# Kernel tuning notes

Measured on AMD Instinct MI355X. Metric: run time of the kernel, lower is better.

The kernel has to match this reference:

```python
import jax, jax.numpy as jnp
import numpy as np

N_NODES = 50000
N_EDGES = 800000
F_IN, C1, C2 = 128, 100, 4
NEG_SLOPE = 0.2  # PyG GATConv default LeakyReLU slope


def setup_inputs() -> dict:
    key = jax.random.key(0)
    ks = jax.random.split(key, 10)
    def glorot(k, shape):
        fan = sum(shape)
        return jax.random.normal(k, shape, jnp.float32) * jnp.sqrt(2.0 / fan)
    return {
        "x": jax.random.normal(ks[0], (N_NODES, F_IN), jnp.float32),
        "edge_index": jax.random.randint(ks[1], (2, N_EDGES), 0, N_NODES, jnp.int64),
        "W1": glorot(ks[2], (F_IN, C1)),
        "att_src1": glorot(ks[3], (1, C1)),
        "att_dst1": glorot(ks[4], (1, C1)),
        "b1": jnp.zeros((C1,), jnp.float32),
        "W2": glorot(ks[5], (C1, C2)),
        "att_src2": glorot(ks[6], (1, C2)),
        "att_dst2": glorot(ks[7], (1, C2)),
        "b2": jnp.zeros((C2,), jnp.float32),
    }


def _gat_conv(x, edge_index, W, att_src, att_dst, bias):
    """PyG GATConv (heads=1, concat=True, add_self_loops=True), eval mode."""
    n = x.shape[0]
    # add self loops
    loop = jnp.arange(n, dtype=edge_index.dtype)
    src = jnp.concatenate([edge_index[0], loop])
    dst = jnp.concatenate([edge_index[1], loop])
    h = x @ W                                   # [N, C]
    a_src = (h * att_src[0]).sum(-1)            # [N]
    a_dst = (h * att_dst[0]).sum(-1)            # [N]
    e = jax.nn.leaky_relu(a_src[src] + a_dst[dst], NEG_SLOPE)  # [E+N]
    # segment softmax over destination neighborhoods
    m = jax.ops.segment_max(e, dst, num_segments=n)            # [N]
    w = jnp.exp(e - m[dst])
    denom = jax.ops.segment_sum(w, dst, num_segments=n)        # [N]
    alpha = w / denom[dst]                                     # [E+N]
    msg = h[src] * alpha[:, None]                              # [E+N, C]
    out = jax.ops.segment_sum(msg, dst, num_segments=n)        # [N, C]
    return out + bias


def reference(x, edge_index, W1, att_src1, att_dst1, b1, W2, att_src2, att_dst2, b2):
    h = _gat_conv(x, edge_index, W1, att_src1, att_dst1, b1)
    h = jax.nn.relu(h)  # dropout is identity in eval mode
    h = _gat_conv(h, edge_index, W2, att_src2, att_dst2, b2)
    return jax.nn.log_softmax(h, axis=1)
```

## Files before the change

### kernel.cpp

```cpp
#include <hip/hip_runtime.h>
#include <math.h>

#define N_NODES 50000
#define N_EDGES 800000
#define F_IN 128
#define C1 100
#define C1D 50
#define C2 4
#define NEG 0.2f
#define DEGCAP 64
#define NBUCK 196
#define BCAP 4608
#define BSTR 16
#define PA_NB 196
#define PA_CHUNK 1021
#define GEMM_NB 782
#define NB_PREP 56
#define AGG1_NB 2048
#define AGG1_NW (AGG1_NB * 4)

typedef __attribute__((ext_vector_type(8))) _Float16 f16x8;
typedef __attribute__((ext_vector_type(2))) _Float16 f16x2;
typedef __attribute__((ext_vector_type(4))) float f32x4;

__device__ __forceinline__ float leaky(float v) { return v > 0.f ? v : NEG * v; }

__device__ __forceinline__ unsigned pkh(float a, float b) {
    auto p = __builtin_amdgcn_cvt_pkrtz(a, b);
    return __builtin_bit_cast(unsigned, p);
}
__device__ __forceinline__ float h_lo(unsigned g) {
    f16x2 p = __builtin_bit_cast(f16x2, g);
    return (float)p[0];
}
__device__ __forceinline__ float h_hi(unsigned g) {
    f16x2 p = __builtin_bit_cast(f16x2, g);
    return (float)p[1];
}

__global__ __launch_bounds__(256) void k_prep(int* __restrict__ bcnt, const float* __restrict__ W1,
                                              unsigned short* __restrict__ W1h) {
    int i = blockIdx.x * 256 + threadIdx.x;
    if (i < NBUCK) bcnt[i * BSTR] = 0;
    if (i < 12800) {
        int k = i / 100, n = i - k * 100;
        _Float16 hv = (_Float16)W1[i];
        W1h[n * 128 + k] = __builtin_bit_cast(unsigned short, hv);
    } else if (i < 12800 + 12 * 128) {
        int e = i - 12800;
        int n = 100 + (e >> 7), k = e & 127;
        W1h[n * 128 + k] = 0;
    }
}

__global__ __launch_bounds__(256)
void k_gemm_scatter(const float* __restrict__ x, const unsigned short* __restrict__ W1h,
                    const float* __restrict__ as1, const float* __restrict__ ad1,
                    unsigned* __restrict__ h1b, float* __restrict__ a_src1,
                    float* __restrict__ a_dst1, const int* __restrict__ ei,
                    int* __restrict__ bcnt, unsigned* __restrict__ breg) {
    if (blockIdx.x < PA_NB) {
        __shared__ int lcnt[NBUCK];
        __shared__ int lbase[NBUCK];
        int tid = threadIdx.x;
        if (tid < NBUCK) lcnt[tid] = 0;
        __syncthreads();
        int g0 = blockIdx.x * PA_CHUNK;
        int4 s4[4], d4[4];
        int off[4][4];
        bool val[4];
#pragma unroll
        for (int it = 0; it < 4; ++it) {
            int local = it * 256 + tid;
            int g = g0 + local;
            val[it] = (local < PA_CHUNK) && (g < N_EDGES / 4);
            if (val[it]) {
                s4[it] = *(const int4*)(ei + (long)g * 4);
                d4[it] = *(const int4*)(ei + N_EDGES + (long)g * 4);
                off[it][0] = atomicAdd(&lcnt[d4[it].x >> 8], 1);
                off[it][1] = atomicAdd(&lcnt[d4[it].y >> 8], 1);
                off[it][2] = atomicAdd(&lcnt[d4[it].z >> 8], 1);
                off[it][3] = atomicAdd(&lcnt[d4[it].w >> 8], 1);
            }
        }
        __syncthreads();
        if (tid < NBUCK) {
            int c = lcnt[tid];
            lbase[tid] = c ? atomicAdd(&bcnt[tid * BSTR], c) : 0;
        }
        __syncthreads();
#pragma unroll
        for (int it = 0; it < 4; ++it) {
            if (!val[it]) continue;
            { int b = d4[it].x >> 8; int p = lbase[b] + off[it][0];
              if (p < BCAP) breg[b * BCAP + p] = ((unsigned)s4[it].x << 8) | ((unsigned)d4[it].x & 255u); }
            { int b = d4[it].y >> 8; int p = lbase[b] + off[it][1];
              if (p < BCAP) breg[b * BCAP + p] = ((unsigned)s4[it].y << 8) | ((unsigned)d4[it].y & 255u); }
            { int b = d4[it].z >> 8; int p = lbase[b] + off[it][2];
              if (p < BCAP) breg[b * BCAP + p] = ((unsigned)s4[it].z << 8) | ((unsigned)d4[it].z & 255u); }
            { int b = d4[it].w >> 8; int p = lbase[b] + off[it][3];
              if (p < BCAP) breg[b * BCAP + p] = ((unsigned)s4[it].w << 8) | ((unsigned)d4[it].w & 255u); }
        }
        return;
    }
    int half = blockIdx.x - PA_NB;
    int tid = threadIdx.x;
    int node0 = half * 64;
    int wave = tid >> 6, lane = tid & 63;
    int mrow = lane & 15;
    int quad = lane >> 4;
    int na = node0 + wave * 16 + mrow;
    bool vrow = na < N_NODES;
    const float* px = x + (long)na * F_IN + quad * 8;

    f16x8 afr[4];
#pragma unroll
    for (int kc = 0; kc < 4; ++kc) {
        float4 v0 = make_float4(0.f, 0.f, 0.f, 0.f), v1 = v0;
        if (vrow) {
            v0 = *(const float4*)(px + kc * 32);
            v1 = *(const float4*)(px + kc * 32 + 4);
        }
        union { unsigned u[4]; f16x8 h; } t;
        t.u[0] = pkh(v0.x, v0.y);
        t.u[1] = pkh(v0.z, v0.w);
        t.u[2] = pkh(v1.x, v1.y);
        t.u[3] = pkh(v1.z, v1.w);
        afr[kc] = t.h;
    }

    f32x4 acc[7];
#pragma unroll
    for (int nt = 0; nt < 7; ++nt) {
        const _Float16* pb = (const _Float16*)W1h + (nt * 16 + mrow) * 128 + quad * 8;
        f32x4 a = {0.f, 0.f, 0.f, 0.f};
#pragma unroll
        for (int kc = 0; kc < 4; ++kc) {
            f16x8 bfr = *(const f16x8*)(pb + kc * 32);
            a = __builtin_amdgcn_mfma_f32_16x16x32_f16(afr[kc], bfr, a, 0, 0, 0);
        }
        acc[nt] = a;
    }

    float ps[4] = {0.f, 0.f, 0.f, 0.f}, pd[4] = {0.f, 0.f, 0.f, 0.f};
#pragma unroll
    for (int nt = 0; nt < 7; ++nt) {
        int col = nt * 16 + mrow;
        float av = 0.f, dv = 0.f;
        if (col < C1) { av = as1[col]; dv = ad1[col]; }
#pragma unroll
        for (int r = 0; r < 4; ++r) {
            ps[r] += acc[nt][r] * av;
            pd[r] += acc[nt][r] * dv;
        }
    }
#pragma unroll
    for (int r = 0; r < 4; ++r) {
#pragma unroll
        for (int off = 1; off < 16; off <<= 1) {
            ps[r] += __shfl_xor(ps[r], off);
            pd[r] += __shfl_xor(pd[r], off);
        }
    }
    if (mrow == 0) {
#pragma unroll
        for (int r = 0; r < 4; ++r) {
            int n = node0 + wave * 16 + quad * 4 + r;
            if (n < N_NODES) { a_src1[n] = ps[r]; a_dst1[n] = pd[r]; }
        }
    }

#pragma unroll
    for (int nt = 0; nt < 7; ++nt) {
#pragma unroll
        for (int r = 0; r < 4; ++r) {
            float v = acc[nt][r];
            float o = __shfl_xor(v, 1);
            int col = nt * 16 + mrow;
            int n = node0 + wave * 16 + quad * 4 + r;
            if ((mrow & 1) == 0 && col < C1 && n < N_NODES) {
                h1b[(long)n * C1D + (col >> 1)] = pkh(v, o);
            }
        }
    }
}

__global__ __launch_bounds__(512) void k_bucket(const unsigned* __restrict__ breg,
                                                const int* __restrict__ bcnt,
                                                int* __restrict__ cnt,
                                                unsigned short* __restrict__ slots) {
    __shared__ int dcnt[256];
    int b = blockIdx.x, tid = threadIdx.x;
    if (tid < 256) dcnt[tid] = 0;
    __syncthreads();
    int n = min(bcnt[b * BSTR], BCAP);
    const unsigned* reg = breg + b * BCAP;
    for (int e = tid; e < n; e += 512) {
        unsigned p = reg[e];
        int d8 = p & 255;
        int slot = atomicAdd(&dcnt[d8], 1);
        if (slot < DEGCAP) slots[(((b << 8) + d8) << 6) + slot] = (unsigned short)(p >> 8);
    }
    __syncthreads();
    if (tid < 256) {
        int d = (b << 8) + tid;
        if (d < N_NODES) cnt[d] = dcnt[tid];
    }
}

__device__ __forceinline__ float rlanef(float v, int l) {
    return __int_as_float(__builtin_amdgcn_readlane(__float_as_int(v), l));
}

__global__ __launch_bounds__(256) void k_agg1(const unsigned* __restrict__ h1b, const float* __restrict__ a_src,
                                              const float* __restrict__ a_dst, const int* __restrict__ cnt,
                                              const unsigned short* __restrict__ slots, const float* __restrict__ b1,
                                              const float* __restrict__ W2, const float* __restrict__ as2,
                                              const float* __restrict__ ad2, float4* __restrict__ h2,
                                              float* __restrict__ a_src2, float* __restrict__ a_dst2) {
    int tid = threadIdx.x;
    int wave = tid >> 6, lane = tid & 63;
    int wid = blockIdx.x * 4 + wave;
    bool act = lane < C1D;
    int cc = act ? lane : 0;

    int d = wid;
    if (d >= N_NODES) return;
    int cnC = min(cnt[d], DEGCAP);
    int sregC = (int)slots[d * DEGCAP + lane];
    float adC = a_dst[d];
    float asdC = a_src[d];

    while (true) {
        int dn = d + AGG1_NW;
        int cnN = 0, sregN = 0; float adN = 0.f, asdN = 0.f;
        if (dn < N_NODES) {
            cnN = min(cnt[dn], DEGCAP);
            sregN = (int)slots[dn * DEGCAP + lane];
            adN = a_dst[dn];
            asdN = a_src[dn];
        }
        int cn = cnC; float ad = adC;
        float asg = a_src[sregC];
        unsigned gs = h1b[(long)d * C1D + cc];
        unsigned ga[8], gb[8];
#define LD(buf, e) { int sv_ = __builtin_amdgcn_readlane(sregC, (e)); \
                     buf = h1b[(long)sv_ * C1D + cc]; }
#define CONSUME(buf, e) if ((e) < cn) { float w_ = rlanef(wreg, (e)); \
                     accL = fmaf(h_lo(buf), w_, accL); accH = fmaf(h_hi(buf), w_, accH); }
#pragma unroll
        for (int i = 0; i < 8; ++i) LD(ga[i], i);
        float wself = __expf(leaky(asdC + ad));
        float wreg = __expf(leaky(asg + ad));
        float lsum = (lane == 0) ? wself : 0.f;
        if (lane < cn) lsum += wreg;
        float accL = wself * h_lo(gs), accH = wself * h_hi(gs);
#pragma unroll
        for (int bp = 0; bp < 4; ++bp) {
            const int b0 = 2 * bp, b1i = 2 * bp + 1;
            if (b0 * 8 >= cn) break;
            if (b1i * 8 < cn) {
#pragma unroll
                for (int i = 0; i < 8; ++i) LD(gb[i], b1i * 8 + i);
            }
#pragma unroll
            for (int i = 0; i < 8; ++i) CONSUME(ga[i], b0 * 8 + i);
            if (b1i * 8 >= cn) break;
            if ((b1i + 1) * 8 < cn) {
#pragma unroll
                for (int i = 0; i < 8; ++i) LD(ga[i], (b1i + 1) * 8 + i);
            }
#pragma unroll
            for (int i = 0; i < 8; ++i) CONSUME(gb[i], b1i * 8 + i);
        }
#undef LD
#undef CONSUME

        for (int off = 32; off; off >>= 1) lsum += __shfl_xor(lsum, off);
        float invl = 1.f / lsum;
        float p0 = 0.f, p1 = 0.f, p2 = 0.f, p3 = 0.f;
        if (act) {
            float v0 = fmaxf(accL * invl + b1[2 * lane], 0.f);
            float v1 = fmaxf(accH * invl + b1[2 * lane + 1], 0.f);
            const float* w0 = W2 + (2 * lane) * 4;
            p0 = v0 * w0[0] + v1 * w0[4];
            p1 = v0 * w0[1] + v1 * w0[5];
            p2 = v0 * w0[2] + v1 * w0[6];
            p3 = v0 * w0[3] + v1 * w0[7];
        }
        for (int off = 32; off; off >>= 1) {
            p0 += __shfl_xor(p0, off);
            p1 += __shfl_xor(p1, off);
            p2 += __shfl_xor(p2, off);
            p3 += __shfl_xor(p3, off);
        }
        if (lane == 0) {
            h2[d] = make_float4(p0, p1, p2, p3);
            a_src2[d] = p0 * as2[0] + p1 * as2[1] + p2 * as2[2] + p3 * as2[3];
            a_dst2[d] = p0 * ad2[0] + p1 * ad2[1] + p2 * ad2[2] + p3 * ad2[3];
        }
        if (dn >= N_NODES) break;
        d = dn; cnC = cnN; sregC = sregN; adC = adN; asdC = asdN;
    }
}

__global__ __launch_bounds__(256) void k_agg2(const float4* __restrict__ h2, const float* __restrict__ a_src,
                                              const float* __restrict__ a_dst, const int* __restrict__ cnt,
                                              const unsigned short* __restrict__ slots, const float* __restrict__ b2,
                                              float4* __restrict__ out) {
    int wave = threadIdx.x >> 6, lane = threadIdx.x & 63;
    int grp = lane >> 4, li = lane & 15;
    for (int d = blockIdx.x * 16 + wave * 4 + grp; d < N_NODES; d += gridDim.x * 16) {
        int cn = min(cnt[d], DEGCAP);
        float ad = a_dst[d];
        float l = 0.f, a0 = 0.f, a1 = 0.f, a2 = 0.f, a3 = 0.f;
        if (li == 0) {
            float w = __expf(leaky(a_src[d] + ad));
            float4 hv = h2[d];
            l = w; a0 = w * hv.x; a1 = w * hv.y; a2 = w * hv.z; a3 = w * hv.w;
        }
        for (int j = li; j < cn; j += 16) {
            int s = (int)slots[d * DEGCAP + j];
            float w = __expf(leaky(a_src[s] + ad));
            l += w;
            float4 hv = h2[s];
            a0 += w * hv.x; a1 += w * hv.y; a2 += w * hv.z; a3 += w * hv.w;
        }
#pragma unroll
        for (int off = 8; off; off >>= 1) {
            l += __shfl_xor(l, off);
            a0 += __shfl_xor(a0, off);
            a1 += __shfl_xor(a1, off);
            a2 += __shfl_xor(a2, off);
            a3 += __shfl_xor(a3, off);
        }
        if (li == 0) {
            float invl = 1.f / l;
            float v0 = a0 * invl + b2[0];
            float v1 = a1 * invl + b2[1];
            float v2 = a2 * invl + b2[2];
            float v3 = a3 * invl + b2[3];
            float mm = fmaxf(fmaxf(v0, v1), fmaxf(v2, v3));
            float ls = logf(__expf(v0 - mm) + __expf(v1 - mm) + __expf(v2 - mm) + __expf(v3 - mm)) + mm;
            out[d] = make_float4(v0 - ls, v1 - ls, v2 - ls, v3 - ls);
        }
    }
}

extern "C" void kernel_launch(void* const* d_in, const int* in_sizes, int n_in,
                              void* d_out, int out_size, void* d_ws, size_t ws_size,
                              hipStream_t stream) {
    const float* x   = (const float*)d_in[0];
    const int*   ei  = (const int*)d_in[1];
    const float* W1  = (const float*)d_in[2];
    const float* as1 = (const float*)d_in[3];
    const float* ad1 = (const float*)d_in[4];
    const float* b1  = (const float*)d_in[5];
    const float* W2  = (const float*)d_in[6];
    const float* as2 = (const float*)d_in[7];
    const float* ad2 = (const float*)d_in[8];
    const float* b2  = (const float*)d_in[9];
    float4* out = (float4*)d_out;

    char* w = (char*)d_ws;
    unsigned* h1b    = (unsigned*)(w + 0);
    float*    a_src1 = (float*)(w + 10000000);
    float*    a_dst1 = (float*)(w + 10200000);
    float4*   h2     = (float4*)(w + 10400000);
    float*    a_src2 = (float*)(w + 11200000);
    float*    a_dst2 = (float*)(w + 11400000);
    int*      cnt    = (int*)(w + 11600000);
    int*      bcnt   = (int*)(w + 11800000);
    unsigned short* slots = (unsigned short*)(w + 11816000);
    unsigned* breg   = (unsigned*)(w + 18216000);
    unsigned short* W1h   = (unsigned short*)(w + 21828672);

    k_prep<<<NB_PREP, 256, 0, stream>>>(bcnt, W1, W1h);
    k_gemm_scatter<<<PA_NB + GEMM_NB, 256, 0, stream>>>(x, W1h, as1, ad1, h1b, a_src1, a_dst1,
                                                        ei, bcnt, breg);
    k_bucket<<<NBUCK, 512, 0, stream>>>(breg, bcnt, cnt, slots);
    k_agg1<<<AGG1_NB, 256, 0, stream>>>(h1b, a_src1, a_dst1, cnt, slots, b1, W2, as2, ad2,
                                        h2, a_src2, a_dst2);
    k_agg2<<<1563, 256, 0, stream>>>(h2, a_src2, a_dst2, cnt, slots, b2, out);
}
```

Baseline: 170.2 us.

## Fuse bucket build into agg1 and stage W1 conversion in shared memory

Removes the k_prep kernel: each GEMM block now converts W1 to fp16 into padded LDS itself, and bcnt is zeroed with a memset. The k_bucket kernel is merged into k_agg1, which now runs one 1024-thread block per 256-node bucket, builds neighbor slots in LDS and aggregates directly from them, while still writing slots/cnt to global for agg2. This cuts launches and global round-trips, but agg1 now runs on only 196 blocks (low occupancy on a large GPU), and every GEMM block redundantly converts W1.

```diff
diff --git a/kernel.cpp b/kernel.cpp
--- a/kernel.cpp
+++ b/kernel.cpp
@@ -15,9 +15,7 @@
 #define PA_NB 196
 #define PA_CHUNK 1021
 #define GEMM_NB 782
-#define NB_PREP 56
-#define AGG1_NB 2048
-#define AGG1_NW (AGG1_NB * 4)
+#define W1P 136
 
 typedef __attribute__((ext_vector_type(8))) _Float16 f16x8;
 typedef __attribute__((ext_vector_type(2))) _Float16 f16x2;
@@ -37,32 +35,24 @@
     f16x2 p = __builtin_bit_cast(f16x2, g);
     return (float)p[1];
 }
-
-__global__ __launch_bounds__(256) void k_prep(int* __restrict__ bcnt, const float* __restrict__ W1,
-                                              unsigned short* __restrict__ W1h) {
-    int i = blockIdx.x * 256 + threadIdx.x;
-    if (i < NBUCK) bcnt[i * BSTR] = 0;
-    if (i < 12800) {
-        int k = i / 100, n = i - k * 100;
-        _Float16 hv = (_Float16)W1[i];
-        W1h[n * 128 + k] = __builtin_bit_cast(unsigned short, hv);
-    } else if (i < 12800 + 12 * 128) {
-        int e = i - 12800;
-        int n = 100 + (e >> 7), k = e & 127;
-        W1h[n * 128 + k] = 0;
-    }
+__device__ __forceinline__ float rlanef(float v, int l) {
+    return __int_as_float(__builtin_amdgcn_readlane(__float_as_int(v), l));
 }
 
 __global__ __launch_bounds__(256)
-void k_gemm_scatter(const float* __restrict__ x, const unsigned short* __restrict__ W1h,
+void k_gemm_scatter(const float* __restrict__ x, const float* __restrict__ W1,
                     const float* __restrict__ as1, const float* __restrict__ ad1,
                     unsigned* __restrict__ h1b, float* __restrict__ a_src1,
                     float* __restrict__ a_dst1, const int* __restrict__ ei,
                     int* __restrict__ bcnt, unsigned* __restrict__ breg) {
+    __shared__ union SM {
+        struct { int lcnt[NBUCK]; int lbase[NBUCK]; } pa;
+        unsigned short w1[112 * W1P];
+    } sm;
+    int tid = threadIdx.x;
     if (blockIdx.x < PA_NB) {
-        __shared__ int lcnt[NBUCK];
-        __shared__ int lbase[NBUCK];
-        int tid = threadIdx.x;
+        int* lcnt = sm.pa.lcnt;
+        int* lbase = sm.pa.lbase;
         if (tid < NBUCK) lcnt[tid] = 0;
         __syncthreads();
         int g0 = blockIdx.x * PA_CHUNK;
@@ -103,8 +93,19 @@
         }
         return;
     }
+    unsigned short* w1s = sm.w1;
+    for (int i = tid; i < 12800; i += 256) {
+        int k = i / 100, n = i - k * 100;
+        _Float16 hv = (_Float16)W1[i];
+        w1s[n * W1P + k] = __builtin_bit_cast(unsigned short, hv);
+    }
+    for (int i = tid; i < 12 * 128; i += 256) {
+        int n = 100 + (i >> 7), k = i & 127;
+        w1s[n * W1P + k] = 0;
+    }
+    __syncthreads();
+
     int half = blockIdx.x - PA_NB;
-    int tid = threadIdx.x;
     int node0 = half * 64;
     int wave = tid >> 6, lane = tid & 63;
     int mrow = lane & 15;
@@ -132,7 +133,7 @@
     f32x4 acc[7];
 #pragma unroll
     for (int nt = 0; nt < 7; ++nt) {
-        const _Float16* pb = (const _Float16*)W1h + (nt * 16 + mrow) * 128 + quad * 8;
+        const _Float16* pb = (const _Float16*)w1s + (nt * 16 + mrow) * W1P + quad * 8;
         f32x4 a = {0.f, 0.f, 0.f, 0.f};
 #pragma unroll
         for (int kc = 0; kc < 4; ++kc) {
@@ -185,122 +186,124 @@
     }
 }
 
-__global__ __launch_bounds__(512) void k_bucket(const unsigned* __restrict__ breg,
-                                                const int* __restrict__ bcnt,
-                                                int* __restrict__ cnt,
-                                                unsigned short* __restrict__ slots) {
+__global__ __launch_bounds__(1024) void k_agg1(const unsigned* __restrict__ h1b, const float* __restrict__ a_src,
+                                               const float* __restrict__ a_dst, const int* __restrict__ bcnt,
+                                               const unsigned* __restrict__ breg, const float* __restrict__ b1,
+                                               const float* __restrict__ W2, const float* __restrict__ as2,
+                                               const float* __restrict__ ad2, float4* __restrict__ h2,
+                                               float* __restrict__ a_src2, float* __restrict__ a_dst2,
+                                               int* __restrict__ cnt_g, unsigned short* __restrict__ slots_g) {
+    __shared__ unsigned short slds[256 * DEGCAP];
     __shared__ int dcnt[256];
     int b = blockIdx.x, tid = threadIdx.x;
     if (tid < 256) dcnt[tid] = 0;
     __syncthreads();
     int n = min(bcnt[b * BSTR], BCAP);
     const unsigned* reg = breg + b * BCAP;
-    for (int e = tid; e < n; e += 512) {
+    for (int e = tid; e < n; e += 1024) {
         unsigned p = reg[e];
         int d8 = p & 255;
         int slot = atomicAdd(&dcnt[d8], 1);
-        if (slot < DEGCAP) slots[(((b << 8) + d8) << 6) + slot] = (unsigned short)(p >> 8);
+        if (slot < DEGCAP) slds[(d8 << 6) + slot] = (unsigned short)(p >> 8);
     }
     __syncthreads();
     if (tid < 256) {
         int d = (b << 8) + tid;
-        if (d < N_NODES) cnt[d] = dcnt[tid];
-    }
-}
-
-__device__ __forceinline__ float rlanef(float v, int l) {
-    return __int_as_float(__builtin_amdgcn_readlane(__float_as_int(v), l));
-}
-
-__global__ __launch_bounds__(256) void k_agg1(const unsigned* __restrict__ h1b, const float* __restrict__ a_src,
-                                              const float* __restrict__ a_dst, const int* __restrict__ cnt,
-                                              const unsigned short* __restrict__ slots, const float* __restrict__ b1,
-                                              const float* __restrict__ W2, const float* __restrict__ as2,
-                                              const float* __restrict__ ad2, float4* __restrict__ h2,
-                                              float* __restrict__ a_src2, float* __restrict__ a_dst2) {
-    int tid = threadIdx.x;
+        if (d < N_NODES) cnt_g[d] = min(dcnt[tid], DEGCAP);
+    }
+    {
+        const uint4* s4 = (const uint4*)slds;
+        uint4* g4 = (uint4*)(slots_g + ((long)b << 14));
+        g4[tid] = s4[tid];
+        g4[tid + 1024] = s4[tid + 1024];
+    }
+
     int wave = tid >> 6, lane = tid & 63;
-    int wid = blockIdx.x * 4 + wave;
     bool act = lane < C1D;
     int cc = act ? lane : 0;
-
-    int d = wid;
-    if (d >= N_NODES) return;
-    int cnC = min(cnt[d], DEGCAP);
-    int sregC = (int)slots[d * DEGCAP + lane];
-    float adC = a_dst[d];
-    float asdC = a_src[d];
-
-    while (true) {
-        int dn = d + AGG1_NW;
+    int base = b << 8;
+
+    int d8C = wave * 16;
+    int dC = base + d8C;
+    bool vC = dC < N_NODES;
+    int cnC = 0, sregC = 0; float adC = 0.f, asdC = 0.f;
+    if (vC) {
+        cnC = min(dcnt[d8C], DEGCAP);
+        sregC = (int)slds[(d8C << 6) + lane];
+        adC = a_dst[dC]; asdC = a_src[dC];
+    }
+    for (int i = 0; i < 16; ++i) {
+        int d8N = d8C + 1;
+        int dN = dC + 1;
+        bool vN = (i < 15) && (dN < N_NODES);
         int cnN = 0, sregN = 0; float adN = 0.f, asdN = 0.f;
-        if (dn < N_NODES) {
-            cnN = min(cnt[dn], DEGCAP);
-            sregN = (int)slots[dn * DEGCAP + lane];
-            adN = a_dst[dn];
-            asdN = a_src[dn];
-        }
-        int cn = cnC; float ad = adC;
-        float asg = a_src[sregC];
-        unsigned gs = h1b[(long)d * C1D + cc];
-        unsigned ga[8], gb[8];
+        if (vN) {
+            cnN = min(dcnt[d8N], DEGCAP);
+            sregN = (int)slds[(d8N << 6) + lane];
+            adN = a_dst[dN]; asdN = a_src[dN];
+        }
+        if (vC) {
+            int cn = cnC; float ad = adC;
+            float asg = a_src[sregC];
+            unsigned gs = h1b[(long)dC * C1D + cc];
+            unsigned ga[8], gb[8];
 #define LD(buf, e) { int sv_ = __builtin_amdgcn_readlane(sregC, (e)); \
                      buf = h1b[(long)sv_ * C1D + cc]; }
 #define CONSUME(buf, e) if ((e) < cn) { float w_ = rlanef(wreg, (e)); \
                      accL = fmaf(h_lo(buf), w_, accL); accH = fmaf(h_hi(buf), w_, accH); }
 #pragma unroll
-        for (int i = 0; i < 8; ++i) LD(ga[i], i);
-        float wself = __expf(leaky(asdC + ad));
-        float wreg = __expf(leaky(asg + ad));
-        float lsum = (lane == 0) ? wself : 0.f;
-        if (lane < cn) lsum += wreg;
-        float accL = wself * h_lo(gs), accH = wself * h_hi(gs);
-#pragma unroll
-        for (int bp = 0; bp < 4; ++bp) {
-            const int b0 = 2 * bp, b1i = 2 * bp + 1;
-            if (b0 * 8 >= cn) break;
-            if (b1i * 8 < cn) {
-#pragma unroll
-                for (int i = 0; i < 8; ++i) LD(gb[i], b1i * 8 + i);
-            }
-#pragma unroll
-            for (int i = 0; i < 8; ++i) CONSUME(ga[i], b0 * 8 + i);
-            if (b1i * 8 >= cn) break;
-            if ((b1i + 1) * 8 < cn) {
-#pragma unroll
-                for (int i = 0; i < 8; ++i) LD(ga[i], (b1i + 1) * 8 + i);
-            }
-#pragma unroll
-            for (int i = 0; i < 8; ++i) CONSUME(gb[i], b1i * 8 + i);
-        }
+            for (int j = 0; j < 8; ++j) LD(ga[j], j);
+            float wself = __expf(leaky(asdC + ad));
+            float wreg = __expf(leaky(asg + ad));
+            float lsum = (lane == 0) ? wself : 0.f;
+            if (lane < cn) lsum += wreg;
+            float accL = wself * h_lo(gs), accH = wself * h_hi(gs);
+#pragma unroll
+            for (int bp = 0; bp < 4; ++bp) {
+                const int b0 = 2 * bp, b1i = 2 * bp + 1;
+                if (b0 * 8 >= cn) break;
+                if (b1i * 8 < cn) {
+#pragma unroll
+                    for (int j = 0; j < 8; ++j) LD(gb[j], b1i * 8 + j);
+                }
+#pragma unroll
+                for (int j = 0; j < 8; ++j) CONSUME(ga[j], b0 * 8 + j);
+                if (b1i * 8 >= cn) break;
+                if ((b1i + 1) * 8 < cn) {
+#pragma unroll
+                    for (int j = 0; j < 8; ++j) LD(ga[j], (b1i + 1) * 8 + j);
+                }
+#pragma unroll
+                for (int j = 0; j < 8; ++j) CONSUME(gb[j], b1i * 8 + j);
+            }
 #undef LD
 #undef CONSUME
 
-        for (int off = 32; off; off >>= 1) lsum += __shfl_xor(lsum, off);
-        float invl = 1.f / lsum;
-        float p0 = 0.f, p1 = 0.f, p2 = 0.f, p3 = 0.f;
-        if (act) {
-            float v0 = fmaxf(accL * invl + b1[2 * lane], 0.f);
-            float v1 = fmaxf(accH * invl + b1[2 * lane + 1], 0.f);
-            const float* w0 = W2 + (2 * lane) * 4;
-            p0 = v0 * w0[0] + v1 * w0[4];
-            p1 = v0 * w0[1] + v1 * w0[5];
-            p2 = v0 * w0[2] + v1 * w0[6];
-            p3 = v0 * w0[3] + v1 * w0[7];
-        }
-        for (int off = 32; off; off >>= 1) {
-            p0 += __shfl_xor(p0, off);
-            p1 += __shfl_xor(p1, off);
-            p2 += __shfl_xor(p2, off);
-            p3 += __shfl_xor(p3, off);
-        }
-        if (lane == 0) {
-            h2[d] = make_float4(p0, p1, p2, p3);
-            a_src2[d] = p0 * as2[0] + p1 * as2[1] + p2 * as2[2] + p3 * as2[3];
-            a_dst2[d] = p0 * ad2[0] + p1 * ad2[1] + p2 * ad2[2] + p3 * ad2[3];
-        }
-        if (dn >= N_NODES) break;
-        d = dn; cnC = cnN; sregC = sregN; adC = adN; asdC = asdN;
+            for (int off = 32; off; off >>= 1) lsum += __shfl_xor(lsum, off);
+            float invl = 1.f / lsum;
+            float p0 = 0.f, p1 = 0.f, p2 = 0.f, p3 = 0.f;
+            if (act) {
+                float v0 = fmaxf(accL * invl + b1[2 * lane], 0.f);
+                float v1 = fmaxf(accH * invl + b1[2 * lane + 1], 0.f);
+                const float* w0 = W2 + (2 * lane) * 4;
+                p0 = v0 * w0[0] + v1 * w0[4];
+                p1 = v0 * w0[1] + v1 * w0[5];
+                p2 = v0 * w0[2] + v1 * w0[6];
+                p3 = v0 * w0[3] + v1 * w0[7];
+            }
+            for (int off = 32; off; off >>= 1) {
+                p0 += __shfl_xor(p0, off);
+                p1 += __shfl_xor(p1, off);
+                p2 += __shfl_xor(p2, off);
+                p3 += __shfl_xor(p3, off);
+            }
+            if (lane == 0) {
+                h2[dC] = make_float4(p0, p1, p2, p3);
+                a_src2[dC] = p0 * as2[0] + p1 * as2[1] + p2 * as2[2] + p3 * as2[3];
+                a_dst2[dC] = p0 * ad2[0] + p1 * ad2[1] + p2 * ad2[2] + p3 * ad2[3];
+            }
+        }
+        d8C = d8N; dC = dN; vC = vN; cnC = cnN; sregC = sregN; adC = adN; asdC = asdN;
     }
 }
 
@@ -373,13 +376,11 @@
     int*      bcnt   = (int*)(w + 11800000);
     unsigned short* slots = (unsigned short*)(w + 11816000);
     unsigned* breg   = (unsigned*)(w + 18216000);
-    unsigned short* W1h   = (unsigned short*)(w + 21828672);
-
-    k_prep<<<NB_PREP, 256, 0, stream>>>(bcnt, W1, W1h);
-    k_gemm_scatter<<<PA_NB + GEMM_NB, 256, 0, stream>>>(x, W1h, as1, ad1, h1b, a_src1, a_dst1,
+
+    hipMemsetAsync(bcnt, 0, NBUCK * BSTR * 4, stream);
+    k_gemm_scatter<<<PA_NB + GEMM_NB, 256, 0, stream>>>(x, W1, as1, ad1, h1b, a_src1, a_dst1,
                                                         ei, bcnt, breg);
-    k_bucket<<<NBUCK, 512, 0, stream>>>(breg, bcnt, cnt, slots);
-    k_agg1<<<AGG1_NB, 256, 0, stream>>>(h1b, a_src1, a_dst1, cnt, slots, b1, W2, as2, ad2,
-                                        h2, a_src2, a_dst2);
+    k_agg1<<<NBUCK, 1024, 0, stream>>>(h1b, a_src1, a_dst1, bcnt, breg, b1, W2, as2, ad2,
+                                       h2, a_src2, a_dst2, cnt, slots);
     k_agg2<<<1563, 256, 0, stream>>>(h2, a_src2, a_dst2, cnt, slots, b2, out);
 }
```

Result: slower. 174.5 us (+2.5%).
